# Performance work log

Hardware: AMD Instinct MI355X
Metric: run time of the kernel (lower is better)

Reference implementation:

```python
import jax, jax.numpy as jnp
import numpy as np

BASE_WEIGHT = 0.01
ADAPTATION_RATE = 0.1
EPS = 1e-8
N = 16384
H = 64


def setup_inputs() -> dict:
    key = jax.random.key(0)
    k1, k2, k3, k4 = jax.random.split(key, 4)
    return {
        "x_input": jax.random.normal(k1, (N,), dtype=jnp.float32),
        "targets": jax.random.normal(k2, (N,), dtype=jnp.float32),
        "w1": jax.random.normal(k3, (H,), dtype=jnp.float32) * 0.5,
        "b1": jnp.zeros((H,), dtype=jnp.float32),
        "w2": jax.random.normal(k4, (H,), dtype=jnp.float32) * 0.5,
        "b2": jnp.zeros((1,), dtype=jnp.float32),
    }


def _mlp(x, w1, b1, w2, b2):
    # elementwise 1 -> H -> 1 tanh MLP: predictions y_i = f(x_i)
    h = jnp.tanh(x[:, None] * w1 + b1)  # [N, H]
    return h @ w2 + b2[0]               # [N]


def _local_density(x):
    # NxN pairwise abs-diff matrix, top-3 smallest per row
    diff = jnp.abs(x[:, None] - x[None, :]) + EPS       # [N, N]
    neg_knn, _ = jax.lax.top_k(-diff, 3)                # smallest 3 via negation
    knn = -neg_knn                                       # [N, 3]
    dens = 1.0 / (knn.mean(axis=1, keepdims=True) + EPS)  # [N, 1]
    return dens / (dens.max() + EPS)


def reference(x_input, targets, w1, b1, w2, b2):
    f_sum = lambda xx: jnp.sum(_mlp(xx, w1, b1, w2, b2))
    predictions = _mlp(x_input, w1, b1, w2, b2)
    mse_loss = jnp.mean((predictions - targets) ** 2)

    # torch.autograd.grad(..., grad_outputs=ones) twice == grad of summed output twice
    dy_dx_sum = lambda xx: jnp.sum(jax.grad(f_sum)(xx))
    d2y_dx2 = jax.grad(dy_dx_sum)(x_input)               # [N]

    density = _local_density(x_input)                    # [N, 1]
    adaptive_weights = 1.0 + ADAPTATION_RATE * density   # [N, 1]
    # torch broadcasts [N,1]*[N] -> [N,N]; mean of that outer product equals
    # mean(weights) * mean(d2**2) exactly, so compute it without the NxN alloc.
    curvature_penalty = BASE_WEIGHT * (jnp.mean(adaptive_weights) * jnp.mean(d2y_dx2 ** 2))

    total_loss = mse_loss + curvature_penalty
    return (total_loss, mse_loss, curvature_penalty)
```

## Files before the change

kernel.cpp:

```cpp
#include <hip/hip_runtime.h>
#include <math.h>

#define NPTS 16384
#define HDIM 64
#define JCH 8
#define CHUNK (NPTS / JCH)
#define IBLK 256
#define EPSF 1e-8f
#define FMAX3 3.402823466e38f

__device__ __forceinline__ void ins3(float& m1, float& m2, float& m3, float d) {
    m3 = __builtin_amdgcn_fmed3f(d, m2, m3);
    m2 = __builtin_amdgcn_fmed3f(d, m1, m2);
    m1 = fminf(d, m1);
}

__global__ __launch_bounds__(IBLK) void knn_partial_kernel(
    const float* __restrict__ x, float* __restrict__ part, float* __restrict__ acc) {
    __shared__ float4 sx[CHUNK / 4];
    const int jc = blockIdx.x & (JCH - 1);
    const int ic = blockIdx.x >> 3;
    const float4* xg = (const float4*)(x + jc * CHUNK);
    for (int t = threadIdx.x; t < CHUNK / 4; t += IBLK) sx[t] = xg[t];
    if (blockIdx.x == 0 && threadIdx.x < 4) acc[threadIdx.x] = 0.0f;
    __syncthreads();

    const int i = ic * IBLK + threadIdx.x;
    const float xi = x[i];
    float a1 = FMAX3, a2 = FMAX3, a3 = FMAX3;
    float c1 = FMAX3, c2 = FMAX3, c3 = FMAX3;
#pragma unroll 4
    for (int k = 0; k < CHUNK / 4; ++k) {
        float4 v = sx[k];
        float d0 = fabsf(xi - v.x);
        float d1 = fabsf(xi - v.y);
        float d2 = fabsf(xi - v.z);
        float d3 = fabsf(xi - v.w);
        ins3(a1, a2, a3, d0);
        ins3(c1, c2, c3, d1);
        ins3(a1, a2, a3, d2);
        ins3(c1, c2, c3, d3);
    }
    ins3(a1, a2, a3, c1);
    ins3(a1, a2, a3, c2);
    ins3(a1, a2, a3, c3);
    part[(jc * 3 + 0) * NPTS + i] = a1;
    part[(jc * 3 + 1) * NPTS + i] = a2;
    part[(jc * 3 + 2) * NPTS + i] = a3;
}

__global__ __launch_bounds__(64) void fuse_kernel(
    const float* __restrict__ x, const float* __restrict__ tg,
    const float* __restrict__ w1, const float* __restrict__ b1,
    const float* __restrict__ w2, const float* __restrict__ b2,
    const float* __restrict__ part, float* __restrict__ acc) {
    __shared__ float sw1[HDIM], sb1[HDIM], sw2[HDIM], sc[HDIM];
    const int t = threadIdx.x;
    sw1[t] = w1[t];
    sb1[t] = b1[t];
    sw2[t] = w2[t];
    sc[t] = w2[t] * w1[t] * w1[t];
    __syncthreads();

    const int i = blockIdx.x * 64 + t;

    float m1 = FMAX3, m2 = FMAX3, m3 = FMAX3;
#pragma unroll
    for (int jc = 0; jc < JCH; ++jc) {
        float p1 = part[(jc * 3 + 0) * NPTS + i];
        float p2 = part[(jc * 3 + 1) * NPTS + i];
        float p3 = part[(jc * 3 + 2) * NPTS + i];
        ins3(m1, m2, m3, p1);
        ins3(m1, m2, m3, p2);
        ins3(m1, m2, m3, p3);
    }
    float sum3 = m1 + m2 + m3;
    float dens = 1.0f / (sum3 * (1.0f / 3.0f) + 2.0f * EPSF);

    const float xi = x[i];
    float y = b2[0];
    float d2a = 0.0f;
#pragma unroll 8
    for (int j = 0; j < HDIM; ++j) {
        float u = fmaf(xi, sw1[j], sb1[j]);
        float e = __expf(2.0f * u);
        float r = __builtin_amdgcn_rcpf(e + 1.0f);
        float tt = fmaf(-2.0f, r, 1.0f);
        y = fmaf(sw2[j], tt, y);
        float s = tt * tt;
        float g = 2.0f * tt * (s - 1.0f);
        d2a = fmaf(sc[j], g, d2a);
    }
    float diff = y - tg[i];
    float msep = diff * diff;
    float d2sq = d2a * d2a;

    float rs_mse = msep, rs_d2 = d2sq, rs_dn = dens, rmx = dens;
    for (int o = 32; o > 0; o >>= 1) {
        rs_mse += __shfl_down(rs_mse, o);
        rs_d2 += __shfl_down(rs_d2, o);
        rs_dn += __shfl_down(rs_dn, o);
        rmx = fmaxf(rmx, __shfl_down(rmx, o));
    }
    if (t == 0) {
        atomicAdd(&acc[0], rs_mse);
        atomicAdd(&acc[1], rs_d2);
        atomicAdd(&acc[2], rs_dn);
        atomicMax((unsigned int*)&acc[3], __float_as_uint(rmx));
    }
}

__global__ void finalize_kernel(const float* __restrict__ acc, float* __restrict__ out) {
    float mse = acc[0] * (1.0f / NPTS);
    float md2 = acc[1] * (1.0f / NPTS);
    float dmax = acc[3];
    float mean_density = (acc[2] * (1.0f / NPTS)) / (dmax + EPSF);
    float mean_w = 1.0f + 0.1f * mean_density;
    float penalty = 0.01f * mean_w * md2;
    out[0] = mse + penalty;
    out[1] = mse;
    out[2] = penalty;
}

extern "C" void kernel_launch(void* const* d_in, const int* in_sizes, int n_in,
                              void* d_out, int out_size, void* d_ws, size_t ws_size,
                              hipStream_t stream) {
    const float* x = (const float*)d_in[0];
    const float* tg = (const float*)d_in[1];
    const float* w1 = (const float*)d_in[2];
    const float* b1 = (const float*)d_in[3];
    const float* w2 = (const float*)d_in[4];
    const float* b2 = (const float*)d_in[5];
    float* out = (float*)d_out;
    float* wsf = (float*)d_ws;
    float* part = wsf;
    float* acc = wsf + JCH * 3 * NPTS;

    hipLaunchKernelGGL(knn_partial_kernel, dim3((NPTS / IBLK) * JCH), dim3(IBLK), 0, stream,
                       x, part, acc);
    hipLaunchKernelGGL(fuse_kernel, dim3(NPTS / 64), dim3(64), 0, stream,
                       x, tg, w1, b1, w2, b2, part, acc);
    hipLaunchKernelGGL(finalize_kernel, dim3(1), dim3(1), 0, stream, acc, out);
}
```

Measured before the change: 112.8 us.

## Read kNN chunk via scalar loads, double j-chunks, fold finalize into fuse kernel

The kNN partial kernel drops its LDS staging and sync and reads the chunk straight from global memory. Because the address is uniform across the wavefront, those reads can become scalar/broadcast loads. The number of j-chunks doubles to 16, giving more blocks and shorter loops, at the cost of more partial results to write and later merge. The finalize kernel is removed: the last block, found with an atomic ticket counter and a threadfence, computes the outputs, which saves one kernel launch.

```diff
diff --git a/kernel.cpp b/kernel.cpp
--- a/kernel.cpp
+++ b/kernel.cpp
@@ -3,7 +3,7 @@
 
 #define NPTS 16384
 #define HDIM 64
-#define JCH 8
+#define JCH 16
 #define CHUNK (NPTS / JCH)
 #define IBLK 256
 #define EPSF 1e-8f
@@ -17,29 +17,21 @@
 
 __global__ __launch_bounds__(IBLK) void knn_partial_kernel(
     const float* __restrict__ x, float* __restrict__ part, float* __restrict__ acc) {
-    __shared__ float4 sx[CHUNK / 4];
     const int jc = blockIdx.x & (JCH - 1);
-    const int ic = blockIdx.x >> 3;
-    const float4* xg = (const float4*)(x + jc * CHUNK);
-    for (int t = threadIdx.x; t < CHUNK / 4; t += IBLK) sx[t] = xg[t];
-    if (blockIdx.x == 0 && threadIdx.x < 4) acc[threadIdx.x] = 0.0f;
-    __syncthreads();
+    const int ic = blockIdx.x >> 4;
+    if (blockIdx.x == 0 && threadIdx.x < 8) acc[threadIdx.x] = 0.0f;
 
     const int i = ic * IBLK + threadIdx.x;
     const float xi = x[i];
+    const float* __restrict__ xc = x + jc * CHUNK;
     float a1 = FMAX3, a2 = FMAX3, a3 = FMAX3;
     float c1 = FMAX3, c2 = FMAX3, c3 = FMAX3;
-#pragma unroll 4
-    for (int k = 0; k < CHUNK / 4; ++k) {
-        float4 v = sx[k];
-        float d0 = fabsf(xi - v.x);
-        float d1 = fabsf(xi - v.y);
-        float d2 = fabsf(xi - v.z);
-        float d3 = fabsf(xi - v.w);
+#pragma unroll 8
+    for (int k = 0; k < CHUNK; k += 2) {
+        float d0 = fabsf(xi - xc[k]);
+        float d1 = fabsf(xi - xc[k + 1]);
         ins3(a1, a2, a3, d0);
         ins3(c1, c2, c3, d1);
-        ins3(a1, a2, a3, d2);
-        ins3(c1, c2, c3, d3);
     }
     ins3(a1, a2, a3, c1);
     ins3(a1, a2, a3, c2);
@@ -53,7 +45,8 @@
     const float* __restrict__ x, const float* __restrict__ tg,
     const float* __restrict__ w1, const float* __restrict__ b1,
     const float* __restrict__ w2, const float* __restrict__ b2,
-    const float* __restrict__ part, float* __restrict__ acc) {
+    const float* __restrict__ part, float* __restrict__ acc,
+    float* __restrict__ out) {
     __shared__ float sw1[HDIM], sb1[HDIM], sw2[HDIM], sc[HDIM];
     const int t = threadIdx.x;
     sw1[t] = w1[t];
@@ -107,19 +100,23 @@
         atomicAdd(&acc[1], rs_d2);
         atomicAdd(&acc[2], rs_dn);
         atomicMax((unsigned int*)&acc[3], __float_as_uint(rmx));
+        __threadfence();
+        unsigned int ticket = atomicAdd((unsigned int*)&acc[4], 1u);
+        if (ticket == gridDim.x - 1) {
+            float s_mse = atomicAdd(&acc[0], 0.0f);
+            float s_d2 = atomicAdd(&acc[1], 0.0f);
+            float s_dn = atomicAdd(&acc[2], 0.0f);
+            float dmax = __uint_as_float(atomicMax((unsigned int*)&acc[3], 0u));
+            float mse = s_mse * (1.0f / NPTS);
+            float md2 = s_d2 * (1.0f / NPTS);
+            float mean_density = (s_dn * (1.0f / NPTS)) / (dmax + EPSF);
+            float mean_w = 1.0f + 0.1f * mean_density;
+            float penalty = 0.01f * mean_w * md2;
+            out[0] = mse + penalty;
+            out[1] = mse;
+            out[2] = penalty;
+        }
     }
-}
-
-__global__ void finalize_kernel(const float* __restrict__ acc, float* __restrict__ out) {
-    float mse = acc[0] * (1.0f / NPTS);
-    float md2 = acc[1] * (1.0f / NPTS);
-    float dmax = acc[3];
-    float mean_density = (acc[2] * (1.0f / NPTS)) / (dmax + EPSF);
-    float mean_w = 1.0f + 0.1f * mean_density;
-    float penalty = 0.01f * mean_w * md2;
-    out[0] = mse + penalty;
-    out[1] = mse;
-    out[2] = penalty;
 }
 
 extern "C" void kernel_launch(void* const* d_in, const int* in_sizes, int n_in,
@@ -139,6 +136,5 @@
     hipLaunchKernelGGL(knn_partial_kernel, dim3((NPTS / IBLK) * JCH), dim3(IBLK), 0, stream,
                        x, part, acc);
     hipLaunchKernelGGL(fuse_kernel, dim3(NPTS / 64), dim3(64), 0, stream,
-                       x, tg, w1, b1, w2, b2, part, acc);
-    hipLaunchKernelGGL(finalize_kernel, dim3(1), dim3(1), 0, stream, acc, out);
+                       x, tg, w1, b1, w2, b2, part, acc, out);
 }
```

Result: no change. 111.8 us (-0.9%).
